# Kernel optimization log

Hardware: AMD Instinct MI355X
Metric: run time of the kernel (lower is better)

Reference implementation:

```python
import jax, jax.numpy as jnp
import numpy as np

B, S, D = 16, 4096, 128
LN_EPS = 1e-5
REC_EPS = 1e-8


def setup_inputs() -> dict:
    key = jax.random.key(0)
    k1, k2, k3, k4 = jax.random.split(key, 4)
    return {
        "C": jax.random.normal(k1, (B, S, D), dtype=jnp.float32),
        "V": jax.random.normal(k2, (B, S, D), dtype=jnp.float32),
        "W": jax.random.normal(k3, (B, S, D), dtype=jnp.float32),
        "encoder_context": jax.random.normal(k4, (B, D), dtype=jnp.float32),
        "time_modulation": jnp.full((1, 1, D), 0.5, dtype=jnp.float32),
        "context_modulation": jnp.full((1, D), 0.5, dtype=jnp.float32),
        "ln_weight": jnp.ones((D,), dtype=jnp.float32),
        "ln_bias": jnp.zeros((D,), dtype=jnp.float32),
    }


def reference(C, V, W, encoder_context, time_modulation, context_modulation, ln_weight, ln_bias):
    b_, s_, d_ = C.shape
    tm = time_modulation[0, 0]  # [D]
    # context gate is time-invariant: compute once
    ctx_add = jax.nn.sigmoid(encoder_context * context_modulation) * encoder_context  # [B,D]

    def step(carry, xs):
        a, bst = carry  # a: [B,1], bst: [B,D]
        c_t, v_t, w_t = xs  # each [B,D]
        decay = jax.nn.sigmoid(w_t * tm)  # [B,D]
        ec = jnp.exp(c_t)  # [B,D]
        a = decay.mean(axis=1, keepdims=True) * a + ec.sum(axis=1, keepdims=True)
        bst = decay * bst + ec * v_t + ctx_add
        out_t = bst / (a + REC_EPS)
        return (a, bst), out_t

    a0 = jnp.zeros((b_, 1), dtype=C.dtype)
    b0 = jnp.zeros((b_, d_), dtype=C.dtype)
    xs = (jnp.swapaxes(C, 0, 1), jnp.swapaxes(V, 0, 1), jnp.swapaxes(W, 0, 1))  # [S,B,D]
    _, ys = jax.lax.scan(step, (a0, b0), xs)  # ys: [S,B,D]
    res = jnp.swapaxes(ys, 0, 1)  # [B,S,D]

    mu = jnp.mean(res, axis=-1, keepdims=True)
    var = jnp.var(res, axis=-1, keepdims=True)
    normed = (res - mu) * jax.lax.rsqrt(var + LN_EPS)
    return normed * ln_weight + ln_bias
```

## Files before the change

### kernel.cpp

```cpp
#include <hip/hip_runtime.h>

#define BB   16
#define SS   4096
#define DD   128
#define NCH  512
#define TT   (SS / NCH)
#define WPB  4
#define NTHR 256

#define DTILE 16
#define SUBS  16
#define CPS   (NCH / SUBS)

#define LN_EPS  1e-5f
#define REC_EPS 1e-8f

__device__ __forceinline__ float fast_rcp(float x) { return __builtin_amdgcn_rcpf(x); }
__device__ __forceinline__ float sigm(float x) { return fast_rcp(1.0f + __expf(-x)); }

__device__ __forceinline__ unsigned pack2(float a, float b) {
    unsigned ua = (__float_as_uint(a) + 0x8000u) >> 16;
    unsigned ub = (__float_as_uint(b) + 0x8000u) & 0xFFFF0000u;
    return ub | ua;
}
__device__ __forceinline__ float up_lo(unsigned u) { return __uint_as_float(u << 16); }
__device__ __forceinline__ float up_hi(unsigned u) { return __uint_as_float(u & 0xFFFF0000u); }

template<int CTRL>
__device__ __forceinline__ float dpp_mov0(float x) {
    return __int_as_float(
        __builtin_amdgcn_update_dpp(0, __float_as_int(x), CTRL, 0xF, 0xF, true));
}

__device__ __forceinline__ void wave_red2(float& a, float& b) {
    a += dpp_mov0<0x111>(a); b += dpp_mov0<0x111>(b);
    a += dpp_mov0<0x112>(a); b += dpp_mov0<0x112>(b);
    a += dpp_mov0<0x114>(a); b += dpp_mov0<0x114>(b);
    a += dpp_mov0<0x118>(a); b += dpp_mov0<0x118>(b);
    a += dpp_mov0<0x142>(a); b += dpp_mov0<0x142>(b);
    a += dpp_mov0<0x143>(a); b += dpp_mov0<0x143>(b);
    a = __int_as_float(__builtin_amdgcn_readlane(__float_as_int(a), 63));
    b = __int_as_float(__builtin_amdgcn_readlane(__float_as_int(b), 63));
}

#define LOAD_FENCE() asm volatile("" ::: "memory")

__global__ __launch_bounds__(NTHR, 4) void pass1_kernel(
    const float* __restrict__ C, const float* __restrict__ V, const float* __restrict__ W,
    const float* __restrict__ enc, const float* __restrict__ tmod, const float* __restrict__ cmod,
    unsigned* __restrict__ DTb,
    float* __restrict__ Pbuf, float* __restrict__ Qbuf,
    float* __restrict__ PaBuf, float* __restrict__ QaBuf,
    float2* __restrict__ MEbuf)
{
    const int wv   = threadIdx.x >> 6;
    const int lane = threadIdx.x & 63;
    const int gc   = blockIdx.x * WPB + wv;
    const int b    = gc >> 9;
    const int ch   = gc & (NCH - 1);
    const int d2   = lane << 1;

    const int t0 = ch * TT;
    const size_t base = ((size_t)b * SS + t0) * DD + d2;
    const float2* Cp = (const float2*)(C + base);
    const float2* Vp = (const float2*)(V + base);
    const float2* Wp = (const float2*)(W + base);
    uint2* DTp = (uint2*)(DTb + base);

    const float2 tm = *(const float2*)(tmod + d2);
    const float2 cm = *(const float2*)(cmod + d2);
    const float2 ec = *(const float2*)(enc + b * DD + d2);

    float2 cR[TT], wR[TT], vR[TT];
#pragma unroll
    for (int t = 0; t < TT; ++t) {
        cR[t] = Cp[t * (DD / 2)];
        wR[t] = Wp[t * (DD / 2)];
        vR[t] = Vp[t * (DD / 2)];
    }
    LOAD_FENCE();

    float2 ctx;
    ctx.x = sigm(ec.x * cm.x) * ec.x;
    ctx.y = sigm(ec.y * cm.y) * ec.y;

    float2 P = make_float2(1.f, 1.f);
    float2 Q = make_float2(0.f, 0.f);
    float sdp[TT], sep[TT];

#pragma unroll
    for (int t = 0; t < TT; ++t) {
        float2 dec, e2, T2; uint2 u;
        dec.x = sigm(wR[t].x * tm.x); dec.y = sigm(wR[t].y * tm.y);
        e2.x = __expf(cR[t].x); e2.y = __expf(cR[t].y);
        T2.x = e2.x * vR[t].x + ctx.x;
        T2.y = e2.y * vR[t].y + ctx.y;

        u.x = pack2(dec.x, T2.x); u.y = pack2(dec.y, T2.y);
        DTp[t * (DD / 2)] = u;

        const float dqx = up_lo(u.x), dqy = up_lo(u.y);
        const float tqx = up_hi(u.x), tqy = up_hi(u.y);
        Q.x = dqx * Q.x + tqx;
        Q.y = dqy * Q.y + tqy;
        P.x *= dqx; P.y *= dqy;

        sdp[t] = dec.x + dec.y;
        sep[t] = e2.x + e2.y;
    }

#pragma unroll
    for (int t = 0; t < TT; ++t) wave_red2(sdp[t], sep[t]);

    float pa = 1.f, qa = 0.f;
    float mk = 0.f, ek = 0.f;
#pragma unroll
    for (int t = 0; t < TT; ++t) {
        const float mt = sdp[t] * (1.0f / DD);
        pa *= mt;
        qa = mt * qa + sep[t];
        if (lane == t) { mk = mt; ek = sep[t]; }
    }

    *(float2*)(Pbuf + (size_t)gc * DD + d2) = P;
    *(float2*)(Qbuf + (size_t)gc * DD + d2) = Q;
    if (lane < TT) MEbuf[(size_t)b * SS + t0 + lane] = make_float2(mk, ek);
    if (lane == 0) { PaBuf[gc] = pa; QaBuf[gc] = qa; }
}

__global__ __launch_bounds__(256, 2) void pass2_kernel(
    const float* __restrict__ Pbuf, const float* __restrict__ Qbuf,
    const float* __restrict__ PaBuf, const float* __restrict__ QaBuf,
    float* __restrict__ bst0, float* __restrict__ a0)
{
    const int b   = blockIdx.x >> 3;
    const int dt  = blockIdx.x & 7;
    const int tid = threadIdx.x;
    const int dl  = tid & (DTILE - 1);
    const int sub = tid >> 4;
    const int d   = dt * DTILE + dl;

    __shared__ float cP[SUBS][DTILE], cQ[SUBS][DTILE], ent[SUBS][DTILE];
    __shared__ float sPa[256], sQa[256];

    const int ch0 = sub * CPS;
    const size_t base = ((size_t)b * NCH + ch0) * DD + d;
    float Pr[CPS], Qr[CPS];
    float p = 1.f, q = 0.f;
#pragma unroll
    for (int i = 0; i < CPS; ++i) {
        Pr[i] = Pbuf[base + (size_t)i * DD];
        Qr[i] = Qbuf[base + (size_t)i * DD];
        q = Pr[i] * q + Qr[i];
        p = Pr[i] * p;
    }
    cP[sub][dl] = p; cQ[sub][dl] = q;
    __syncthreads();

    if (tid < DTILE) {
        float s = 0.f;
#pragma unroll
        for (int sb = 0; sb < SUBS; ++sb) {
            ent[sb][tid] = s;
            s = cP[sb][tid] * s + cQ[sb][tid];
        }
    }
    __syncthreads();

    float s = ent[sub][dl];
#pragma unroll
    for (int i = 0; i < CPS; ++i) {
        bst0[base + (size_t)i * DD] = s;
        s = Pr[i] * s + Qr[i];
    }

    if (dt == 0) {
        const int cbase = b * NCH;
        const float p0 = PaBuf[cbase + 2 * tid],     q0 = QaBuf[cbase + 2 * tid];
        const float p1 = PaBuf[cbase + 2 * tid + 1], q1 = QaBuf[cbase + 2 * tid + 1];
        float Pc = p1 * p0;
        float Qc = p1 * q0 + q1;
#pragma unroll
        for (int off = 1; off < 256; off <<= 1) {
            sPa[tid] = Pc; sQa[tid] = Qc;
            __syncthreads();
            if (tid >= off) {
                const float pp = sPa[tid - off], qq = sQa[tid - off];
                Qc = Pc * qq + Qc;
                Pc = Pc * pp;
            }
            __syncthreads();
        }
        sQa[tid] = Qc;
        __syncthreads();
        const float E = (tid == 0) ? 0.f : sQa[tid - 1];
        a0[cbase + 2 * tid]     = E;
        a0[cbase + 2 * tid + 1] = p0 * E + q0;
    }
}

__global__ __launch_bounds__(NTHR, 4) void pass3_kernel(
    const unsigned* __restrict__ DTb,
    const float* __restrict__ lnw, const float* __restrict__ lnb,
    const float* __restrict__ bst0, const float* __restrict__ a0,
    const float2* __restrict__ MEbuf,
    float* __restrict__ out)
{
    const int wv   = threadIdx.x >> 6;
    const int lane = threadIdx.x & 63;
    const int gc   = blockIdx.x * WPB + wv;
    const int b    = gc >> 9;
    const int ch   = gc & (NCH - 1);
    const int d2   = lane << 1;

    const int t0 = ch * TT;
    const size_t base = ((size_t)b * SS + t0) * DD + d2;
    const uint2* DTp = (const uint2*)(DTb + base);
    float2* Op = (float2*)(out + base);

    uint2 dtR[TT];
#pragma unroll
    for (int t = 0; t < TT; ++t) dtR[t] = DTp[t * (DD / 2)];
    const float2 me = MEbuf[(size_t)b * SS + t0 + (lane & (TT - 1))];
    float2 bst = *(const float2*)(bst0 + (size_t)gc * DD + d2);
    const float a_in = a0[gc];
    const float2 gw = *(const float2*)(lnw + d2);
    const float2 gb = *(const float2*)(lnb + d2);
    LOAD_FENCE();

    float a = a_in;
    float2 o[TT];
    float s1p[TT], s2p[TT];
#pragma unroll
    for (int t = 0; t < TT; ++t) {
        const float mt = __int_as_float(__builtin_amdgcn_readlane(__float_as_int(me.x), t));
        const float et = __int_as_float(__builtin_amdgcn_readlane(__float_as_int(me.y), t));

        a = mt * a + et;
        bst.x = up_lo(dtR[t].x) * bst.x + up_hi(dtR[t].x);
        bst.y = up_lo(dtR[t].y) * bst.y + up_hi(dtR[t].y);

        const float inva = fast_rcp(a + REC_EPS);
        o[t].x = bst.x * inva; o[t].y = bst.y * inva;
        s1p[t] = o[t].x + o[t].y;
        s2p[t] = o[t].x * o[t].x + o[t].y * o[t].y;
    }

#pragma unroll
    for (int t = 0; t < TT; ++t) wave_red2(s1p[t], s2p[t]);

#pragma unroll
    for (int t = 0; t < TT; ++t) {
        const float mu  = s1p[t] * (1.0f / DD);
        const float var = s2p[t] * (1.0f / DD) - mu * mu;
        const float rs  = rsqrtf(var + LN_EPS);
        float2 r;
        r.x = (o[t].x - mu) * rs * gw.x + gb.x;
        r.y = (o[t].y - mu) * rs * gw.y + gb.y;
        Op[t * (DD / 2)] = r;
    }
}

extern "C" void kernel_launch(void* const* d_in, const int* in_sizes, int n_in,
                              void* d_out, int out_size, void* d_ws, size_t ws_size,
                              hipStream_t stream)
{
    const float* C    = (const float*)d_in[0];
    const float* V    = (const float*)d_in[1];
    const float* W    = (const float*)d_in[2];
    const float* enc  = (const float*)d_in[3];
    const float* tmod = (const float*)d_in[4];
    const float* cmod = (const float*)d_in[5];
    const float* lnw  = (const float*)d_in[6];
    const float* lnb  = (const float*)d_in[7];
    float* out = (float*)d_out;

    float* ws    = (float*)d_ws;
    unsigned* DTbuf = (unsigned*)ws;
    float* Pbuf  = ws    + (size_t)BB * SS * DD;
    float* Qbuf  = Pbuf  + (size_t)BB * NCH * DD;
    float* bst0  = Qbuf  + (size_t)BB * NCH * DD;
    float2* MEbuf = (float2*)(bst0 + (size_t)BB * NCH * DD);
    float* PaBuf = (float*)(MEbuf + (size_t)BB * SS);
    float* QaBuf = PaBuf + (size_t)BB * NCH;
    float* a0Buf = QaBuf + (size_t)BB * NCH;

    const int nblk = BB * NCH / WPB;
    pass1_kernel<<<nblk, NTHR, 0, stream>>>(C, V, W, enc, tmod, cmod, DTbuf,
                                            Pbuf, Qbuf, PaBuf, QaBuf, MEbuf);
    pass2_kernel<<<BB * 8, 256, 0, stream>>>(Pbuf, Qbuf, PaBuf, QaBuf, bst0, a0Buf);
    pass3_kernel<<<nblk, NTHR, 0, stream>>>(DTbuf, lnw, lnb,
                                            bst0, a0Buf, MEbuf, out);
}
```

Measured before the change: 157.8 us.

## Process four chunks per wave with double-buffered register prefetch in passes 1 and 3

Each wave in pass1 and pass3 now handles four consecutive chunks rather than one. The loads for the next chunk are issued into a second register buffer while the current chunk is computed, so memory latency overlaps with compute inside a wave. This cuts the grid to a quarter of the blocks and lowers the occupancy hint from 4 to 2 blocks per CU to leave room for the larger register footprint. The trade-off is fewer waves to hide latency across, which relies on the in-wave prefetch to cover it.

After: 163.7 us. 3.7% more time.

```diff
diff --git a/kernel.cpp b/kernel.cpp
--- a/kernel.cpp
+++ b/kernel.cpp
@@ -7,6 +7,10 @@
 #define TT   (SS / NCH)
 #define WPB  4
 #define NTHR 256
+#define NWAVE (BB * NCH)
+#define KCH  4
+#define NW1  (NWAVE / KCH)
+#define NBLK1 (NW1 / WPB)
 
 #define DTILE 16
 #define SUBS  16
@@ -43,9 +47,7 @@
     b = __int_as_float(__builtin_amdgcn_readlane(__float_as_int(b), 63));
 }
 
-#define LOAD_FENCE() asm volatile("" ::: "memory")
-
-__global__ __launch_bounds__(NTHR, 4) void pass1_kernel(
+__global__ __launch_bounds__(NTHR, 2) void pass1_kernel(
     const float* __restrict__ C, const float* __restrict__ V, const float* __restrict__ W,
     const float* __restrict__ enc, const float* __restrict__ tmod, const float* __restrict__ cmod,
     unsigned* __restrict__ DTb,
@@ -55,13 +57,13 @@
 {
     const int wv   = threadIdx.x >> 6;
     const int lane = threadIdx.x & 63;
-    const int gc   = blockIdx.x * WPB + wv;
-    const int b    = gc >> 9;
-    const int ch   = gc & (NCH - 1);
+    const int wid  = blockIdx.x * WPB + wv;
+    const int gc0  = wid * KCH;
+    const int b    = gc0 >> 9;
+    const int ch0  = gc0 & (NCH - 1);
     const int d2   = lane << 1;
 
-    const int t0 = ch * TT;
-    const size_t base = ((size_t)b * SS + t0) * DD + d2;
+    const size_t base = ((size_t)b * SS + ch0 * TT) * DD + d2;
     const float2* Cp = (const float2*)(C + base);
     const float2* Vp = (const float2*)(V + base);
     const float2* Wp = (const float2*)(W + base);
@@ -70,62 +72,68 @@
     const float2 tm = *(const float2*)(tmod + d2);
     const float2 cm = *(const float2*)(cmod + d2);
     const float2 ec = *(const float2*)(enc + b * DD + d2);
-
-    float2 cR[TT], wR[TT], vR[TT];
-#pragma unroll
-    for (int t = 0; t < TT; ++t) {
-        cR[t] = Cp[t * (DD / 2)];
-        wR[t] = Wp[t * (DD / 2)];
-        vR[t] = Vp[t * (DD / 2)];
-    }
-    LOAD_FENCE();
-
     float2 ctx;
     ctx.x = sigm(ec.x * cm.x) * ec.x;
     ctx.y = sigm(ec.y * cm.y) * ec.y;
 
-    float2 P = make_float2(1.f, 1.f);
-    float2 Q = make_float2(0.f, 0.f);
-    float sdp[TT], sep[TT];
-
-#pragma unroll
-    for (int t = 0; t < TT; ++t) {
-        float2 dec, e2, T2; uint2 u;
-        dec.x = sigm(wR[t].x * tm.x); dec.y = sigm(wR[t].y * tm.y);
-        e2.x = __expf(cR[t].x); e2.y = __expf(cR[t].y);
-        T2.x = e2.x * vR[t].x + ctx.x;
-        T2.y = e2.y * vR[t].y + ctx.y;
-
-        u.x = pack2(dec.x, T2.x); u.y = pack2(dec.y, T2.y);
-        DTp[t * (DD / 2)] = u;
-
-        const float dqx = up_lo(u.x), dqy = up_lo(u.y);
-        const float tqx = up_hi(u.x), tqy = up_hi(u.y);
-        Q.x = dqx * Q.x + tqx;
-        Q.y = dqy * Q.y + tqy;
-        P.x *= dqx; P.y *= dqy;
-
-        sdp[t] = dec.x + dec.y;
-        sep[t] = e2.x + e2.y;
-    }
-
-#pragma unroll
-    for (int t = 0; t < TT; ++t) wave_red2(sdp[t], sep[t]);
-
-    float pa = 1.f, qa = 0.f;
-    float mk = 0.f, ek = 0.f;
-#pragma unroll
-    for (int t = 0; t < TT; ++t) {
-        const float mt = sdp[t] * (1.0f / DD);
-        pa *= mt;
-        qa = mt * qa + sep[t];
-        if (lane == t) { mk = mt; ek = sep[t]; }
-    }
-
-    *(float2*)(Pbuf + (size_t)gc * DD + d2) = P;
-    *(float2*)(Qbuf + (size_t)gc * DD + d2) = Q;
-    if (lane < TT) MEbuf[(size_t)b * SS + t0 + lane] = make_float2(mk, ek);
-    if (lane == 0) { PaBuf[gc] = pa; QaBuf[gc] = qa; }
+    float2 cA[TT], wA[TT], vA[TT], cB[TT], wB[TT], vB[TT];
+
+#define LD1(X, k) do { \
+    const int off_ = (k) * (TT * DD / 2); \
+    _Pragma("unroll") \
+    for (int t = 0; t < TT; ++t) { \
+        c##X[t] = Cp[off_ + t * (DD / 2)]; \
+        w##X[t] = Wp[off_ + t * (DD / 2)]; \
+        v##X[t] = Vp[off_ + t * (DD / 2)]; \
+    } \
+} while (0)
+
+#define CH1(X, k) do { \
+    float2 P = make_float2(1.f, 1.f), Q = make_float2(0.f, 0.f); \
+    float sdp[TT], sep[TT]; \
+    const int off_ = (k) * (TT * DD / 2); \
+    _Pragma("unroll") \
+    for (int t = 0; t < TT; ++t) { \
+        float2 dec, e2, T2; uint2 u; \
+        dec.x = sigm(w##X[t].x * tm.x); dec.y = sigm(w##X[t].y * tm.y); \
+        e2.x = __expf(c##X[t].x); e2.y = __expf(c##X[t].y); \
+        T2.x = e2.x * v##X[t].x + ctx.x; \
+        T2.y = e2.y * v##X[t].y + ctx.y; \
+        u.x = pack2(dec.x, T2.x); u.y = pack2(dec.y, T2.y); \
+        DTp[off_ + t * (DD / 2)] = u; \
+        const float dqx = up_lo(u.x), dqy = up_lo(u.y); \
+        const float tqx = up_hi(u.x), tqy = up_hi(u.y); \
+        Q.x = dqx * Q.x + tqx; Q.y = dqy * Q.y + tqy; \
+        P.x *= dqx; P.y *= dqy; \
+        sdp[t] = dec.x + dec.y; sep[t] = e2.x + e2.y; \
+    } \
+    _Pragma("unroll") \
+    for (int t = 0; t < TT; ++t) wave_red2(sdp[t], sep[t]); \
+    float pa = 1.f, qa = 0.f, mk = 0.f, ek = 0.f; \
+    _Pragma("unroll") \
+    for (int t = 0; t < TT; ++t) { \
+        const float mt = sdp[t] * (1.0f / DD); \
+        pa *= mt; qa = mt * qa + sep[t]; \
+        if (lane == t) { mk = mt; ek = sep[t]; } \
+    } \
+    const int gc_ = gc0 + (k); \
+    *(float2*)(Pbuf + (size_t)gc_ * DD + d2) = P; \
+    *(float2*)(Qbuf + (size_t)gc_ * DD + d2) = Q; \
+    if (lane < TT) MEbuf[(size_t)b * SS + (ch0 + (k)) * TT + lane] = make_float2(mk, ek); \
+    if (lane == 0) { PaBuf[gc_] = pa; QaBuf[gc_] = qa; } \
+} while (0)
+
+    LD1(A, 0);
+    LD1(B, 1);
+    CH1(A, 0);
+    LD1(A, 2);
+    CH1(B, 1);
+    LD1(B, 3);
+    CH1(A, 2);
+    CH1(B, 3);
+
+#undef LD1
+#undef CH1
 }
 
 __global__ __launch_bounds__(256, 2) void pass2_kernel(
@@ -199,7 +207,7 @@
     }
 }
 
-__global__ __launch_bounds__(NTHR, 4) void pass3_kernel(
+__global__ __launch_bounds__(NTHR, 2) void pass3_kernel(
     const unsigned* __restrict__ DTb,
     const float* __restrict__ lnw, const float* __restrict__ lnb,
     const float* __restrict__ bst0, const float* __restrict__ a0,
@@ -208,57 +216,74 @@
 {
     const int wv   = threadIdx.x >> 6;
     const int lane = threadIdx.x & 63;
-    const int gc   = blockIdx.x * WPB + wv;
-    const int b    = gc >> 9;
-    const int ch   = gc & (NCH - 1);
+    const int wid  = blockIdx.x * WPB + wv;
+    const int gc0  = wid * KCH;
+    const int b    = gc0 >> 9;
+    const int ch0  = gc0 & (NCH - 1);
     const int d2   = lane << 1;
 
-    const int t0 = ch * TT;
-    const size_t base = ((size_t)b * SS + t0) * DD + d2;
+    const size_t base = ((size_t)b * SS + ch0 * TT) * DD + d2;
     const uint2* DTp = (const uint2*)(DTb + base);
     float2* Op = (float2*)(out + base);
 
-    uint2 dtR[TT];
-#pragma unroll
-    for (int t = 0; t < TT; ++t) dtR[t] = DTp[t * (DD / 2)];
-    const float2 me = MEbuf[(size_t)b * SS + t0 + (lane & (TT - 1))];
-    float2 bst = *(const float2*)(bst0 + (size_t)gc * DD + d2);
-    const float a_in = a0[gc];
     const float2 gw = *(const float2*)(lnw + d2);
     const float2 gb = *(const float2*)(lnb + d2);
-    LOAD_FENCE();
-
-    float a = a_in;
-    float2 o[TT];
-    float s1p[TT], s2p[TT];
-#pragma unroll
-    for (int t = 0; t < TT; ++t) {
-        const float mt = __int_as_float(__builtin_amdgcn_readlane(__float_as_int(me.x), t));
-        const float et = __int_as_float(__builtin_amdgcn_readlane(__float_as_int(me.y), t));
-
-        a = mt * a + et;
-        bst.x = up_lo(dtR[t].x) * bst.x + up_hi(dtR[t].x);
-        bst.y = up_lo(dtR[t].y) * bst.y + up_hi(dtR[t].y);
-
-        const float inva = fast_rcp(a + REC_EPS);
-        o[t].x = bst.x * inva; o[t].y = bst.y * inva;
-        s1p[t] = o[t].x + o[t].y;
-        s2p[t] = o[t].x * o[t].x + o[t].y * o[t].y;
-    }
-
-#pragma unroll
-    for (int t = 0; t < TT; ++t) wave_red2(s1p[t], s2p[t]);
-
-#pragma unroll
-    for (int t = 0; t < TT; ++t) {
-        const float mu  = s1p[t] * (1.0f / DD);
-        const float var = s2p[t] * (1.0f / DD) - mu * mu;
-        const float rs  = rsqrtf(var + LN_EPS);
-        float2 r;
-        r.x = (o[t].x - mu) * rs * gw.x + gb.x;
-        r.y = (o[t].y - mu) * rs * gw.y + gb.y;
-        Op[t * (DD / 2)] = r;
-    }
+
+    uint2 dtA[TT], dtB[TT];
+    float2 meA, meB, bstA, bstB;
+    float aA, aB;
+
+#define LD3(X, k) do { \
+    const int off_ = (k) * (TT * DD / 2); \
+    _Pragma("unroll") \
+    for (int t = 0; t < TT; ++t) dt##X[t] = DTp[off_ + t * (DD / 2)]; \
+    me##X  = MEbuf[(size_t)b * SS + (ch0 + (k)) * TT + (lane & (TT - 1))]; \
+    bst##X = *(const float2*)(bst0 + (size_t)(gc0 + (k)) * DD + d2); \
+    a##X   = a0[gc0 + (k)]; \
+} while (0)
+
+#define CH3(X, k) do { \
+    float a = a##X; \
+    float2 bst = bst##X; \
+    float2 o[TT]; float s1p[TT], s2p[TT]; \
+    _Pragma("unroll") \
+    for (int t = 0; t < TT; ++t) { \
+        const float mt = __int_as_float(__builtin_amdgcn_readlane(__float_as_int(me##X.x), t)); \
+        const float et = __int_as_float(__builtin_amdgcn_readlane(__float_as_int(me##X.y), t)); \
+        a = mt * a + et; \
+        bst.x = up_lo(dt##X[t].x) * bst.x + up_hi(dt##X[t].x); \
+        bst.y = up_lo(dt##X[t].y) * bst.y + up_hi(dt##X[t].y); \
+        const float inva = fast_rcp(a + REC_EPS); \
+        o[t].x = bst.x * inva; o[t].y = bst.y * inva; \
+        s1p[t] = o[t].x + o[t].y; \
+        s2p[t] = o[t].x * o[t].x + o[t].y * o[t].y; \
+    } \
+    _Pragma("unroll") \
+    for (int t = 0; t < TT; ++t) wave_red2(s1p[t], s2p[t]); \
+    const int off_ = (k) * (TT * DD / 2); \
+    _Pragma("unroll") \
+    for (int t = 0; t < TT; ++t) { \
+        const float mu  = s1p[t] * (1.0f / DD); \
+        const float var = s2p[t] * (1.0f / DD) - mu * mu; \
+        const float rs  = rsqrtf(var + LN_EPS); \
+        float2 r; \
+        r.x = (o[t].x - mu) * rs * gw.x + gb.x; \
+        r.y = (o[t].y - mu) * rs * gw.y + gb.y; \
+        Op[off_ + t * (DD / 2)] = r; \
+    } \
+} while (0)
+
+    LD3(A, 0);
+    LD3(B, 1);
+    CH3(A, 0);
+    LD3(A, 2);
+    CH3(B, 1);
+    LD3(B, 3);
+    CH3(A, 2);
+    CH3(B, 3);
+
+#undef LD3
+#undef CH3
 }
 
 extern "C" void kernel_launch(void* const* d_in, const int* in_sizes, int n_in,
@@ -285,10 +310,9 @@
     float* QaBuf = PaBuf + (size_t)BB * NCH;
     float* a0Buf = QaBuf + (size_t)BB * NCH;
 
-    const int nblk = BB * NCH / WPB;
-    pass1_kernel<<<nblk, NTHR, 0, stream>>>(C, V, W, enc, tmod, cmod, DTbuf,
-                                            Pbuf, Qbuf, PaBuf, QaBuf, MEbuf);
+    pass1_kernel<<<NBLK1, NTHR, 0, stream>>>(C, V, W, enc, tmod, cmod, DTbuf,
+                                             Pbuf, Qbuf, PaBuf, QaBuf, MEbuf);
     pass2_kernel<<<BB * 8, 256, 0, stream>>>(Pbuf, Qbuf, PaBuf, QaBuf, bst0, a0Buf);
-    pass3_kernel<<<nblk, NTHR, 0, stream>>>(DTbuf, lnw, lnb,
-                                            bst0, a0Buf, MEbuf, out);
-}
+    pass3_kernel<<<NBLK1, NTHR, 0, stream>>>(DTbuf, lnw, lnb,
+                                             bst0, a0Buf, MEbuf, out);
+}
```

## Rewrite chunk-carry scan as per-wave shuffle scan over channels

Applied to the files above, without the earlier changes.

The middle pass of the chunked linear recurrence now assigns one wavefront per (batch, feature) pair. Each lane composes 8 consecutive chunks, then the lanes run a Kogge-Stone scan with warp shuffles. Extra waves do the same for the scalar normaliser carry. This replaces the old 128-block scheme, which used shared-memory serial sub-scans plus a block-wide barrier scan, with about 520 blocks that need no LDS or barriers, giving more parallelism for this latency-bound step. The per-wave loads are strided by D, so coalescing is poorer than the old layout.

After: 174.5 us. +10.6%, slower.

```diff
diff --git a/kernel.cpp b/kernel.cpp
--- a/kernel.cpp
+++ b/kernel.cpp
@@ -7,10 +7,7 @@
 #define TT   (SS / NCH)
 #define WPB  4
 #define NTHR 256
-
-#define DTILE 16
-#define SUBS  16
-#define CPS   (NCH / SUBS)
+#define NWAVE (BB * NCH)
 
 #define LN_EPS  1e-5f
 #define REC_EPS 1e-8f
@@ -128,74 +125,82 @@
     if (lane == 0) { PaBuf[gc] = pa; QaBuf[gc] = qa; }
 }
 
-__global__ __launch_bounds__(256, 2) void pass2_kernel(
+__global__ __launch_bounds__(256, 4) void pass2_kernel(
     const float* __restrict__ Pbuf, const float* __restrict__ Qbuf,
     const float* __restrict__ PaBuf, const float* __restrict__ QaBuf,
     float* __restrict__ bst0, float* __restrict__ a0)
 {
-    const int b   = blockIdx.x >> 3;
-    const int dt  = blockIdx.x & 7;
-    const int tid = threadIdx.x;
-    const int dl  = tid & (DTILE - 1);
-    const int sub = tid >> 4;
-    const int d   = dt * DTILE + dl;
-
-    __shared__ float cP[SUBS][DTILE], cQ[SUBS][DTILE], ent[SUBS][DTILE];
-    __shared__ float sPa[256], sQa[256];
-
-    const int ch0 = sub * CPS;
-    const size_t base = ((size_t)b * NCH + ch0) * DD + d;
-    float Pr[CPS], Qr[CPS];
-    float p = 1.f, q = 0.f;
-#pragma unroll
-    for (int i = 0; i < CPS; ++i) {
-        Pr[i] = Pbuf[base + (size_t)i * DD];
-        Qr[i] = Qbuf[base + (size_t)i * DD];
-        q = Pr[i] * q + Qr[i];
-        p = Pr[i] * p;
-    }
-    cP[sub][dl] = p; cQ[sub][dl] = q;
-    __syncthreads();
-
-    if (tid < DTILE) {
-        float s = 0.f;
-#pragma unroll
-        for (int sb = 0; sb < SUBS; ++sb) {
-            ent[sb][tid] = s;
-            s = cP[sb][tid] * s + cQ[sb][tid];
-        }
-    }
-    __syncthreads();
-
-    float s = ent[sub][dl];
-#pragma unroll
-    for (int i = 0; i < CPS; ++i) {
-        bst0[base + (size_t)i * DD] = s;
-        s = Pr[i] * s + Qr[i];
-    }
-
-    if (dt == 0) {
-        const int cbase = b * NCH;
-        const float p0 = PaBuf[cbase + 2 * tid],     q0 = QaBuf[cbase + 2 * tid];
-        const float p1 = PaBuf[cbase + 2 * tid + 1], q1 = QaBuf[cbase + 2 * tid + 1];
-        float Pc = p1 * p0;
-        float Qc = p1 * q0 + q1;
-#pragma unroll
-        for (int off = 1; off < 256; off <<= 1) {
-            sPa[tid] = Pc; sQa[tid] = Qc;
-            __syncthreads();
-            if (tid >= off) {
-                const float pp = sPa[tid - off], qq = sQa[tid - off];
-                Qc = Pc * qq + Qc;
-                Pc = Pc * pp;
-            }
-            __syncthreads();
-        }
-        sQa[tid] = Qc;
-        __syncthreads();
-        const float E = (tid == 0) ? 0.f : sQa[tid - 1];
-        a0[cbase + 2 * tid]     = E;
-        a0[cbase + 2 * tid + 1] = p0 * E + q0;
+    const int wv   = threadIdx.x >> 6;
+    const int lane = threadIdx.x & 63;
+    const int wid  = blockIdx.x * 4 + wv;
+
+    if (wid < BB * DD) {
+        const int b = wid >> 7;
+        const int d = wid & (DD - 1);
+        const int ch0 = lane * 8;
+        const size_t base = ((size_t)b * NCH + ch0) * DD + d;
+
+        float Ap[8], Aq[8];
+#pragma unroll
+        for (int i = 0; i < 8; ++i) {
+            Ap[i] = Pbuf[base + (size_t)i * DD];
+            Aq[i] = Qbuf[base + (size_t)i * DD];
+        }
+
+        float p = 1.f, q = 0.f;
+#pragma unroll
+        for (int i = 0; i < 8; ++i) { q = Ap[i] * q + Aq[i]; p = Ap[i] * p; }
+
+#pragma unroll
+        for (int dl = 1; dl < 64; dl <<= 1) {
+            float ps = __shfl_up(p, dl);
+            float qs = __shfl_up(q, dl);
+            ps = (lane >= dl) ? ps : 1.f;
+            qs = (lane >= dl) ? qs : 0.f;
+            q = p * qs + q;
+            p = p * ps;
+        }
+
+        float x = __shfl_up(q, 1);
+        x = (lane >= 1) ? x : 0.f;
+
+#pragma unroll
+        for (int i = 0; i < 8; ++i) {
+            bst0[base + (size_t)i * DD] = x;
+            x = Ap[i] * x + Aq[i];
+        }
+    } else if (wid < BB * DD + BB) {
+        const int b = wid - BB * DD;
+        const int ch0 = lane * 8;
+
+        float Ap[8], Aq[8];
+#pragma unroll
+        for (int i = 0; i < 8; ++i) {
+            Ap[i] = PaBuf[b * NCH + ch0 + i];
+            Aq[i] = QaBuf[b * NCH + ch0 + i];
+        }
+
+        float p = 1.f, q = 0.f;
+#pragma unroll
+        for (int i = 0; i < 8; ++i) { q = Ap[i] * q + Aq[i]; p = Ap[i] * p; }
+
+#pragma unroll
+        for (int dl = 1; dl < 64; dl <<= 1) {
+            float ps = __shfl_up(p, dl);
+            float qs = __shfl_up(q, dl);
+            ps = (lane >= dl) ? ps : 1.f;
+            qs = (lane >= dl) ? qs : 0.f;
+            q = p * qs + q;
+            p = p * ps;
+        }
+
+        float x = __shfl_up(q, 1);
+        x = (lane >= 1) ? x : 0.f;
+#pragma unroll
+        for (int i = 0; i < 8; ++i) {
+            a0[b * NCH + ch0 + i] = x;
+            x = Ap[i] * x + Aq[i];
+        }
     }
 }
 
@@ -288,7 +293,8 @@
     const int nblk = BB * NCH / WPB;
     pass1_kernel<<<nblk, NTHR, 0, stream>>>(C, V, W, enc, tmod, cmod, DTbuf,
                                             Pbuf, Qbuf, PaBuf, QaBuf, MEbuf);
-    pass2_kernel<<<BB * 8, 256, 0, stream>>>(Pbuf, Qbuf, PaBuf, QaBuf, bst0, a0Buf);
+    pass2_kernel<<<(BB * DD + BB + 3) / 4, 256, 0, stream>>>(Pbuf, Qbuf, PaBuf, QaBuf,
+                                                             bst0, a0Buf);
     pass3_kernel<<<nblk, NTHR, 0, stream>>>(DTbuf, lnw, lnb,
                                             bst0, a0Buf, MEbuf, out);
 }
```
